# Optimization experiments

Hardware: AMD Instinct MI355X
Metric: run time of the kernel (lower is better)

Reference implementation:

```python
import jax, jax.numpy as jnp
import numpy as np

ALPHA = 1.702  # ORT swiglu activation constant


def setup_inputs() -> dict:
    key = jax.random.key(0)
    ks = jax.random.split(key, 6)
    B, S, H, I, E = 4, 1024, 2048, 2048, 8
    return {
        "hidden_states": jax.random.normal(ks[0], (B, S, H), dtype=jnp.float32),
        "gate_w": jax.random.normal(ks[1], (E, H), dtype=jnp.float32) * 0.02,
        "fc1_w": jax.random.normal(ks[2], (E, 2 * I, H), dtype=jnp.float32) * 0.02,
        "fc1_b": jax.random.normal(ks[3], (E, 2 * I), dtype=jnp.float32) * 0.02,
        "fc2_w": jax.random.normal(ks[4], (E, H, I), dtype=jnp.float32) * 0.02,
        "fc2_b": jax.random.normal(ks[5], (E, H), dtype=jnp.float32) * 0.02,
        "top_k": 2,
    }


def reference(hidden_states, gate_w, fc1_w, fc1_b, fc2_w, fc2_b, top_k):
    B, S, H = hidden_states.shape
    E = gate_w.shape[0]
    x = hidden_states.reshape(-1, H)                      # [T, H]
    T = x.shape[0]

    # Router: softmax -> top-k -> renormalize selected weights
    logits = jnp.einsum("th,eh->te", x, gate_w)           # [T, E]
    probs = jax.nn.softmax(logits, axis=-1)
    top_vals, top_idx = jax.lax.top_k(probs, top_k)       # [T, k]
    top_vals = top_vals / jnp.sum(top_vals, axis=-1, keepdims=True)
    # Dense combine weights [T, E] (zero for non-selected experts)
    combine = jnp.zeros((T, E), dtype=x.dtype).at[
        jnp.arange(T)[:, None], top_idx
    ].add(top_vals)

    # Expert FC1 (packed gate/linear, interleaved) -> swiglu -> FC2
    h = jnp.einsum("th,efh->etf", x, fc1_w) + fc1_b[:, None, :]   # [E, T, 2I]
    g = h[..., 0::2]                                              # gate part [E, T, I]
    l = h[..., 1::2]                                              # linear part [E, T, I]
    a = g * jax.nn.sigmoid(ALPHA * g) * (l + 1.0)                 # [E, T, I]
    y = jnp.einsum("eti,ehi->eth", a, fc2_w) + fc2_b[:, None, :]  # [E, T, H]

    out = jnp.einsum("te,eth->th", combine, y)            # weighted combine
    return out.reshape(B, S, H)
```

## Files before the change

### kernel.cpp

```cpp
#include <hip/hip_runtime.h>
#include <math.h>


#define T_TOK 4096
#define H_DIM 2048
#define I_DIM 2048
#define F_DIM 4096
#define E_NUM 8
#define ALPHA_C 1.702f
#define ALPHA_LOG2E 2.4554674f

#define TILE_M 64
#define KT 32
#define ACT_CAP_F (2 * T_TOK + E_NUM * TILE_M)
#define BTM 128
#define ACT_CAP_B (2 * T_TOK + E_NUM * BTM)

#define GATE_BLOCKS (T_TOK / 4)
#define CHUNK_F4 2048
#define NCHUNK 12288
#define W1_CHUNKS 8192
#define W1_F4 16777216
#define CVT_BLOCKS 2048
#define CVT_ITERS (NCHUNK / CVT_BLOCKS)

typedef unsigned short ushort_t;
typedef __attribute__((ext_vector_type(8))) unsigned short ushort8v;
typedef __attribute__((ext_vector_type(8))) __bf16 bf16x8;
typedef __attribute__((ext_vector_type(4))) float f32x4;

__device__ __forceinline__ ushort_t f2bf(float f) {
    unsigned int u = __float_as_uint(f);
    unsigned int r = (u + 0x7FFFu + ((u >> 16) & 1u)) >> 16;
    return (ushort_t)r;
}
__device__ __forceinline__ float bf2f(ushort_t b) {
    return __uint_as_float(((unsigned int)b) << 16);
}

__device__ __forceinline__ void gl_lds16(const ushort_t* g, ushort_t* l) {
    __builtin_amdgcn_global_load_lds(
        (const __attribute__((address_space(1))) void*)g,
        (__attribute__((address_space(3))) void*)l, 16, 0, 0);
}

__global__ __launch_bounds__(256) void gate_kernel(
    const float* __restrict__ x, const float* __restrict__ gw,
    ushort_t* __restrict__ xb, int4* __restrict__ tidx,
    float2* __restrict__ twgt) {
    int t = blockIdx.x * 4 + (threadIdx.x >> 6);
    int lane = threadIdx.x & 63;
    const float* xr = x + (size_t)t * H_DIM;
    ushort_t* xbr = xb + (size_t)t * H_DIM;
    float acc[E_NUM];
#pragma unroll
    for (int e = 0; e < E_NUM; e++) acc[e] = 0.f;
#pragma unroll
    for (int i = 0; i < H_DIM / 256; i++) {
        int j = (i * 64 + lane) * 4;
        float4 xv = *(const float4*)(xr + j);
        *(ushort4*)(xbr + j) =
            make_ushort4(f2bf(xv.x), f2bf(xv.y), f2bf(xv.z), f2bf(xv.w));
#pragma unroll
        for (int e = 0; e < E_NUM; e++) {
            float4 g = *(const float4*)(gw + e * H_DIM + j);
            acc[e] += xv.x * g.x + xv.y * g.y + xv.z * g.z + xv.w * g.w;
        }
    }
#pragma unroll
    for (int e = 0; e < E_NUM; e++) {
#pragma unroll
        for (int s = 32; s > 0; s >>= 1) acc[e] += __shfl_xor(acc[e], s, 64);
    }
    if (lane == 0) {
        int i0 = 0; float b0 = acc[0];
        for (int e = 1; e < E_NUM; e++) if (acc[e] > b0) { b0 = acc[e]; i0 = e; }
        int i1 = -1; float b1 = -3.0e38f;
        for (int e = 0; e < E_NUM; e++) {
            if (e == i0) continue;
            if (acc[e] > b1) { b1 = acc[e]; i1 = e; }
        }
        float e10 = expf(b1 - b0);
        float w0 = 1.f / (1.f + e10);
        float w1v = 1.f - w0;
        tidx[t] = make_int4(i0, 0, i1, 0);
        twgt[t] = make_float2(w0, w1v);
    }
}

__global__ __launch_bounds__(256) void route_kernel(
    const int4* tidx_ro, int* tidx_w, int* __restrict__ tok,
    int* __restrict__ cnt) {
    int e = blockIdx.x;
    int tid = threadIdx.x;
    int lane = tid & 63;
    int wv = tid >> 6;
    __shared__ int wsum[4];
    __shared__ int sbase;
    if (tid == 0) sbase = 0;
    __syncthreads();
    for (int c = 0; c < T_TOK / 256; c++) {
        int t = c * 256 + tid;
        int4 v = tidx_ro[t];
        bool fA = (v.x == e);
        bool fB = (v.z == e);
        bool f = fA || fB;
        unsigned long long m = __ballot(f);
        int my = __popcll(m & ((1ull << lane) - 1ull));
        int wt = __popcll(m);
        if (lane == 0) wsum[wv] = wt;
        __syncthreads();
        int woff = 0;
#pragma unroll
        for (int q = 0; q < 4; q++) woff += (q < wv) ? wsum[q] : 0;
        int tot = wsum[0] + wsum[1] + wsum[2] + wsum[3];
        int base = sbase;
        if (f) {
            int p = base + woff + my;
            tok[e * T_TOK + p] = t;
            tidx_w[t * 4 + (fA ? 1 : 3)] = p;
        }
        __syncthreads();
        if (tid == 0) sbase = base + tot;
        __syncthreads();
    }
    if (tid == 0) cnt[e] = sbase;
}

__global__ __launch_bounds__(256) void cvt_kernel(
    const float* __restrict__ w1, const float* __restrict__ w2,
    ushort_t* __restrict__ wb) {
    int bid = (int)blockIdx.x;
    int tid = (int)threadIdx.x;
    for (int i = 0; i < CVT_ITERS; i++) {
        int c = bid + i * CVT_BLOCKS;
        size_t g0 = (size_t)c * CHUNK_F4 + tid;
        const float* s = (c < W1_CHUNKS)
                             ? (w1 + g0 * 4)
                             : (w2 + (g0 - (size_t)W1_F4) * 4);
        ushort_t* d = wb + g0 * 4;
        f32x4 v[8];
#pragma unroll
        for (int j = 0; j < 8; j++)
            v[j] = *(const f32x4*)(s + (size_t)j * 1024);
#pragma unroll
        for (int j = 0; j < 8; j++) {
            *(ushort4*)(d + (size_t)j * 1024) = make_ushort4(
                f2bf(v[j][0]), f2bf(v[j][1]), f2bf(v[j][2]), f2bf(v[j][3]));
        }
    }
}

__device__ __forceinline__ void calc_off(const int* __restrict__ cnt, int e,
                                         int& off_e, int& cpad_e) {
    int o = 0, cp = 0;
#pragma unroll
    for (int q = 0; q < E_NUM; q++) {
        int c = (cnt[q] + BTM - 1) & ~(BTM - 1);
        if (q < e) o += c;
        if (q == e) cp = c;
    }
    off_e = o; cpad_e = cp;
}

__global__ __launch_bounds__(256, 3) void fc1_mfma(
    const ushort_t* __restrict__ xb, const ushort_t* __restrict__ w1b,
    const float* __restrict__ b1, const int* __restrict__ tok,
    const int* __restrict__ cnt, ushort_t* __restrict__ act) {
    int e = blockIdx.y >> 5;
    int tile = blockIdx.y & 31;
    int off_e, cpad_e;
    calc_off(cnt, e, off_e, cpad_e);
    if (tile * BTM >= cpad_e) return;
    int i0 = blockIdx.x * 64;

    __shared__ ushort_t As[2][128 * 32];
    __shared__ ushort_t Bg[2][64 * 32];
    __shared__ ushort_t Bl[2][64 * 32];

    int tid = threadIdx.x;
    int lane = tid & 63;
    int ww = tid >> 6;
    int wm = ww & 1, wn = ww >> 1;
    int l15 = lane & 15, quad = lane >> 4;
    int r4 = lane >> 2;
    int koff = (lane & 3) * 8;

    const int* tlist = tok + e * T_TOK + tile * BTM;
    int ar0 = ww * 32 + r4;
    const ushort_t* a0 = xb + (size_t)tlist[ar0] * H_DIM + koff;
    const ushort_t* a1 = xb + (size_t)tlist[ar0 + 16] * H_DIM + koff;
    int il = ww * 16 + r4;
    const ushort_t* bsrc = w1b + ((size_t)e * F_DIM + 2 * (i0 + il)) * H_DIM + koff;

    ushort_t* ad0a = &As[0][(ww * 32) * 32];
    ushort_t* ad0b = &As[0][(ww * 32 + 16) * 32];
    ushort_t* ad1a = &As[1][(ww * 32) * 32];
    ushort_t* ad1b = &As[1][(ww * 32 + 16) * 32];
    ushort_t* bg0 = &Bg[0][(ww * 16) * 32];
    ushort_t* bg1 = &Bg[1][(ww * 16) * 32];
    ushort_t* bl0 = &Bl[0][(ww * 16) * 32];
    ushort_t* bl1 = &Bl[1][(ww * 16) * 32];

    f32x4 zf = {0.f, 0.f, 0.f, 0.f};
    f32x4 accg[4][2], accl[4][2];
#pragma unroll
    for (int mc = 0; mc < 4; mc++)
#pragma unroll
        for (int nc = 0; nc < 2; nc++) { accg[mc][nc] = zf; accl[mc][nc] = zf; }

    for (int k0 = 0; k0 < H_DIM; k0 += 64) {
        __syncthreads();
        gl_lds16(a0, ad0a);
        gl_lds16(a1, ad0b);
        gl_lds16(a0 + 32, ad1a);
        gl_lds16(a1 + 32, ad1b);
        gl_lds16(bsrc, bg0);
        gl_lds16(bsrc + 32, bg1);
        gl_lds16(bsrc + H_DIM, bl0);
        gl_lds16(bsrc + H_DIM + 32, bl1);
        a0 += 64; a1 += 64; bsrc += 64;
        __syncthreads();

#pragma unroll
        for (int kk = 0; kk < 2; kk++) {
            bf16x8 af[4], bgf[2], blf[2];
#pragma unroll
            for (int mc = 0; mc < 4; mc++)
                af[mc] = *(const bf16x8*)&As[kk][(wm * 64 + mc * 16 + l15) * 32 + quad * 8];
#pragma unroll
            for (int nc = 0; nc < 2; nc++) {
                bgf[nc] = *(const bf16x8*)&Bg[kk][(wn * 32 + nc * 16 + l15) * 32 + quad * 8];
                blf[nc] = *(const bf16x8*)&Bl[kk][(wn * 32 + nc * 16 + l15) * 32 + quad * 8];
            }
#pragma unroll
            for (int mc = 0; mc < 4; mc++)
#pragma unroll
                for (int nc = 0; nc < 2; nc++) {
                    accg[mc][nc] = __builtin_amdgcn_mfma_f32_16x16x32_bf16(
                        af[mc], bgf[nc], accg[mc][nc], 0, 0, 0);
                    accl[mc][nc] = __builtin_amdgcn_mfma_f32_16x16x32_bf16(
                        af[mc], blf[nc], accl[mc][nc], 0, 0, 0);
                }
        }
    }

    int rowbase = off_e + tile * BTM + wm * 64;
    int colbase = i0 + wn * 32;
    float bgc[2], blc[2];
#pragma unroll
    for (int nc = 0; nc < 2; nc++) {
        int i = colbase + nc * 16 + l15;
        bgc[nc] = b1[(size_t)e * F_DIM + 2 * i];
        blc[nc] = b1[(size_t)e * F_DIM + 2 * i + 1];
    }
#pragma unroll
    for (int mc = 0; mc < 4; mc++)
#pragma unroll
        for (int nc = 0; nc < 2; nc++) {
            int i = colbase + nc * 16 + l15;
#pragma unroll
            for (int r = 0; r < 4; r++) {
                int m = rowbase + mc * 16 + quad * 4 + r;
                float g = accg[mc][nc][r] + bgc[nc];
                float l = accl[mc][nc][r] + blc[nc];
                float s = __builtin_amdgcn_rcpf(
                    1.f + __builtin_amdgcn_exp2f(-ALPHA_LOG2E * g));
                act[(size_t)m * I_DIM + i] = f2bf(g * s * (l + 1.f));
            }
        }
}

__global__ __launch_bounds__(256, 3) void fc2_mfma(
    const ushort_t* __restrict__ act, const ushort_t* __restrict__ w2b,
    const float* __restrict__ b2, const int* __restrict__ cnt,
    ushort_t* __restrict__ ybuf) {
    int e = blockIdx.y >> 5;
    int tile = blockIdx.y & 31;
    int off_e, cpad_e;
    calc_off(cnt, e, off_e, cpad_e);
    if (tile * BTM >= cpad_e) return;
    int h0 = blockIdx.x * 128;
    int rowbase = off_e + tile * BTM;

    __shared__ ushort_t As[2][128 * 32];
    __shared__ ushort_t Bs[2][128 * 32];

    int tid = threadIdx.x;
    int lane = tid & 63;
    int ww = tid >> 6;
    int wm = ww & 1, wn = ww >> 1;
    int l15 = lane & 15, quad = lane >> 4;
    int r4 = lane >> 2;
    int koff = (lane & 3) * 8;

    int ar = ww * 32 + r4;
    const ushort_t* a0 = act + (size_t)(rowbase + ar) * I_DIM + koff;
    const ushort_t* a1 = a0 + (size_t)16 * I_DIM;
    const ushort_t* b0 = w2b + ((size_t)e * H_DIM + h0 + ar) * I_DIM + koff;
    const ushort_t* b1p = b0 + (size_t)16 * I_DIM;

    ushort_t* ad0a = &As[0][(ww * 32) * 32];
    ushort_t* ad0b = &As[0][(ww * 32 + 16) * 32];
    ushort_t* ad1a = &As[1][(ww * 32) * 32];
    ushort_t* ad1b = &As[1][(ww * 32 + 16) * 32];
    ushort_t* bd0a = &Bs[0][(ww * 32) * 32];
    ushort_t* bd0b = &Bs[0][(ww * 32 + 16) * 32];
    ushort_t* bd1a = &Bs[1][(ww * 32) * 32];
    ushort_t* bd1b = &Bs[1][(ww * 32 + 16) * 32];

    f32x4 zf = {0.f, 0.f, 0.f, 0.f};
    f32x4 acc[4][4];
#pragma unroll
    for (int mc = 0; mc < 4; mc++)
#pragma unroll
        for (int nc = 0; nc < 4; nc++) acc[mc][nc] = zf;

    for (int k0 = 0; k0 < I_DIM; k0 += 64) {
        __syncthreads();
        gl_lds16(a0, ad0a);
        gl_lds16(a1, ad0b);
        gl_lds16(a0 + 32, ad1a);
        gl_lds16(a1 + 32, ad1b);
        gl_lds16(b0, bd0a);
        gl_lds16(b1p, bd0b);
        gl_lds16(b0 + 32, bd1a);
        gl_lds16(b1p + 32, bd1b);
        a0 += 64; a1 += 64; b0 += 64; b1p += 64;
        __syncthreads();

#pragma unroll
        for (int kk = 0; kk < 2; kk++) {
            bf16x8 af[4], bf[4];
#pragma unroll
            for (int mc = 0; mc < 4; mc++)
                af[mc] = *(const bf16x8*)&As[kk][(wm * 64 + mc * 16 + l15) * 32 + quad * 8];
#pragma unroll
            for (int nc = 0; nc < 4; nc++)
                bf[nc] = *(const bf16x8*)&Bs[kk][(wn * 64 + nc * 16 + l15) * 32 + quad * 8];
#pragma unroll
            for (int mc = 0; mc < 4; mc++)
#pragma unroll
                for (int nc = 0; nc < 4; nc++)
                    acc[mc][nc] = __builtin_amdgcn_mfma_f32_16x16x32_bf16(
                        af[mc], bf[nc], acc[mc][nc], 0, 0, 0);
        }
    }

    float bc[4];
#pragma unroll
    for (int nc = 0; nc < 4; nc++)
        bc[nc] = b2[(size_t)e * H_DIM + h0 + wn * 64 + nc * 16 + l15];
#pragma unroll
    for (int mc = 0; mc < 4; mc++)
#pragma unroll
        for (int nc = 0; nc < 4; nc++) {
            int h = h0 + wn * 64 + nc * 16 + l15;
#pragma unroll
            for (int r = 0; r < 4; r++) {
                int m = rowbase + wm * 64 + mc * 16 + quad * 4 + r;
                ybuf[(size_t)m * H_DIM + h] = f2bf(acc[mc][nc][r] + bc[nc]);
            }
        }
}

__global__ __launch_bounds__(256) void combine_kernel(
    const ushort_t* __restrict__ ybuf, const int4* __restrict__ tidx,
    const float2* __restrict__ twgt, const int* __restrict__ cnt,
    float* __restrict__ out) {
    int offv[E_NUM];
    {
        int o = 0;
#pragma unroll
        for (int q = 0; q < E_NUM; q++) {
            offv[q] = o;
            o += (cnt[q] + BTM - 1) & ~(BTM - 1);
        }
    }
    int h = threadIdx.x * 8;
#pragma unroll
    for (int tt = 0; tt < 4; tt++) {
        int t = blockIdx.x * 4 + tt;
        int4 idx = tidx[t];
        float2 w = twgt[t];
        size_t r0 = (size_t)offv[idx.x] + idx.y;
        size_t r1 = (size_t)offv[idx.z] + idx.w;
        ushort8v a = *(const ushort8v*)(ybuf + r0 * H_DIM + h);
        ushort8v b = *(const ushort8v*)(ybuf + r1 * H_DIM + h);
        float* op = out + (size_t)t * H_DIM + h;
#pragma unroll
        for (int q = 0; q < 8; q++)
            op[q] = w.x * bf2f(a[q]) + w.y * bf2f(b[q]);
    }
}

__global__ __launch_bounds__(64) void gate_fb(
    const float* __restrict__ x, const float* __restrict__ gw,
    int* __restrict__ tok, float* __restrict__ wgt,
    int4* __restrict__ tidx, float2* __restrict__ twgt, int* __restrict__ cnt) {
    int t = blockIdx.x;
    int lane = threadIdx.x;
    const float* xr = x + (size_t)t * H_DIM;
    float acc[E_NUM];
#pragma unroll
    for (int e = 0; e < E_NUM; e++) acc[e] = 0.f;
    for (int j = lane; j < H_DIM; j += 64) {
        float xv = xr[j];
#pragma unroll
        for (int e = 0; e < E_NUM; e++) acc[e] += xv * gw[e * H_DIM + j];
    }
#pragma unroll
    for (int e = 0; e < E_NUM; e++) {
#pragma unroll
        for (int s = 32; s > 0; s >>= 1) acc[e] += __shfl_xor(acc[e], s, 64);
    }
    if (lane == 0) {
        int i0 = 0; float b0 = acc[0];
        for (int e = 1; e < E_NUM; e++) if (acc[e] > b0) { b0 = acc[e]; i0 = e; }
        int i1 = -1; float b1 = -3.0e38f;
        for (int e = 0; e < E_NUM; e++) {
            if (e == i0) continue;
            if (acc[e] > b1) { b1 = acc[e]; i1 = e; }
        }
        float e10 = expf(b1 - b0);
        float w0 = 1.f / (1.f + e10);
        float w1 = 1.f - w0;
        int p0 = atomicAdd(&cnt[i0], 1);
        tok[i0 * T_TOK + p0] = t; wgt[i0 * T_TOK + p0] = w0;
        int p1 = atomicAdd(&cnt[i1], 1);
        tok[i1 * T_TOK + p1] = t; wgt[i1 * T_TOK + p1] = w1;
        tidx[t] = make_int4(i0, p0, i1, p1);
        twgt[t] = make_float2(w0, w1);
    }
}

__global__ __launch_bounds__(256) void pad_kernel(
    int* __restrict__ tok, float* __restrict__ wgt,
    const int* __restrict__ cnt, int* __restrict__ cnt_pad,
    int* __restrict__ off, int tile) {
    __shared__ int s_cnt[E_NUM], s_pad[E_NUM];
    if (threadIdx.x == 0) {
        int o = 0;
        for (int e = 0; e < E_NUM; e++) {
            int c = cnt[e];
            int cp = (c + tile - 1) / tile * tile;
            s_cnt[e] = c; s_pad[e] = cp;
            cnt_pad[e] = cp;
            off[e] = o;
            o += cp;
        }
    }
    __syncthreads();
    for (int e = 0; e < E_NUM; e++) {
        for (int p = s_cnt[e] + (int)threadIdx.x; p < s_pad[e]; p += 256) {
            tok[e * T_TOK + p] = 0;
            wgt[e * T_TOK + p] = 0.f;
        }
    }
}

__global__ __launch_bounds__(256) void fc1_kernel(
    const float* __restrict__ x, const float* __restrict__ w1,
    const float* __restrict__ b1, const int* __restrict__ tok,
    const int* __restrict__ cnt_pad, const int* __restrict__ off,
    ushort_t* __restrict__ act) {
    int e = blockIdx.y >> 6;
    int tile = blockIdx.y & 63;
    if (tile * TILE_M >= cnt_pad[e]) return;
    int i0 = blockIdx.x * 64;
    int f0 = i0 * 2;

    __shared__ float xs[KT][TILE_M + 4];
    __shared__ float wsh[KT][128 + 4];

    int tid = threadIdx.x;
    int tx = tid & 15, ty = tid >> 4;
    int rloc = tid >> 3;
    int c4 = (tid & 7) * 4;

    const int* tlist = tok + e * T_TOK + tile * TILE_M;
    int tk0 = tlist[rloc];
    int tk1 = tlist[rloc + 32];
    const float* xp0 = x + (size_t)tk0 * H_DIM + c4;
    const float* xp1 = x + (size_t)tk1 * H_DIM + c4;
    const float* wp = w1 + ((size_t)e * F_DIM + f0 + rloc) * H_DIM + c4;

    float ga[4][4] = {{0.f}}, la[4][4] = {{0.f}};

    for (int k0 = 0; k0 < H_DIM; k0 += KT) {
        __syncthreads();
        {
            float4 v0 = *(const float4*)(xp0 + k0);
            float4 v1 = *(const float4*)(xp1 + k0);
            xs[c4 + 0][rloc] = v0.x; xs[c4 + 1][rloc] = v0.y;
            xs[c4 + 2][rloc] = v0.z; xs[c4 + 3][rloc] = v0.w;
            xs[c4 + 0][rloc + 32] = v1.x; xs[c4 + 1][rloc + 32] = v1.y;
            xs[c4 + 2][rloc + 32] = v1.z; xs[c4 + 3][rloc + 32] = v1.w;
        }
        {
#pragma unroll
            for (int r = 0; r < 4; r++) {
                float4 v = *(const float4*)(wp + (size_t)(32 * r) * H_DIM + k0);
                int fr = rloc + 32 * r;
                wsh[c4 + 0][fr] = v.x; wsh[c4 + 1][fr] = v.y;
                wsh[c4 + 2][fr] = v.z; wsh[c4 + 3][fr] = v.w;
            }
        }
        __syncthreads();
#pragma unroll
        for (int k = 0; k < KT; k++) {
            float4 xv = *(const float4*)&xs[k][ty * 4];
            float4 wa = *(const float4*)&wsh[k][tx * 8];
            float4 wb = *(const float4*)&wsh[k][tx * 8 + 4];
            float xm[4] = {xv.x, xv.y, xv.z, xv.w};
            float gg[4] = {wa.x, wa.z, wb.x, wb.z};
            float ll[4] = {wa.y, wa.w, wb.y, wb.w};
#pragma unroll
            for (int m = 0; m < 4; m++)
#pragma unroll
                for (int n = 0; n < 4; n++) {
                    ga[m][n] += xm[m] * gg[n];
                    la[m][n] += xm[m] * ll[n];
                }
        }
    }

    int rowbase = off[e] + tile * TILE_M;
    float bg[4], bl[4];
#pragma unroll
    for (int n = 0; n < 4; n++) {
        int i = i0 + tx * 4 + n;
        bg[n] = b1[(size_t)e * F_DIM + 2 * i];
        bl[n] = b1[(size_t)e * F_DIM + 2 * i + 1];
    }
#pragma unroll
    for (int m = 0; m < 4; m++) {
        int row = rowbase + ty * 4 + m;
        ushort_t us[4];
#pragma unroll
        for (int n = 0; n < 4; n++) {
            float g = ga[m][n] + bg[n];
            float l = la[m][n] + bl[n];
            float s = 1.f / (1.f + expf(-ALPHA_C * g));
            us[n] = f2bf(g * s * (l + 1.f));
        }
        *(ushort4*)&act[(size_t)row * I_DIM + i0 + tx * 4] =
            make_ushort4(us[0], us[1], us[2], us[3]);
    }
}

__global__ __launch_bounds__(256) void fc2_kernel(
    const ushort_t* __restrict__ act, const float* __restrict__ w2,
    const float* __restrict__ b2, const int* __restrict__ tok,
    const float* __restrict__ wgt, const int* __restrict__ cnt_pad,
    const int* __restrict__ off, float* __restrict__ out) {
    int e = blockIdx.y >> 6;
    int tile = blockIdx.y & 63;
    if (tile * TILE_M >= cnt_pad[e]) return;
    int h0 = blockIdx.x * 64;

    __shared__ float as_[KT][TILE_M + 4];
    __shared__ float wsh[KT][64 + 4];

    int tid = threadIdx.x;
    int tx = tid & 15, ty = tid >> 4;
    int rowbase = off[e] + tile * TILE_M;

    int arow = tid >> 2;
    int ac8 = (tid & 3) * 8;
    const ushort_t* ap = act + (size_t)(rowbase + arow) * I_DIM + ac8;
    int rloc = tid >> 3;
    int c4 = (tid & 7) * 4;
    const float* wp = w2 + ((size_t)e * H_DIM + h0 + rloc) * I_DIM + c4;

    float acc[4][4] = {{0.f}};

    for (int k0 = 0; k0 < I_DIM; k0 += KT) {
        __syncthreads();
        {
            ushort8v v = *(const ushort8v*)(ap + k0);
#pragma unroll
            for (int q = 0; q < 8; q++) as_[ac8 + q][arow] = bf2f(v[q]);
        }
        {
#pragma unroll
            for (int r = 0; r < 2; r++) {
                float4 v = *(const float4*)(wp + (size_t)(32 * r) * I_DIM + k0);
                int hr = rloc + 32 * r;
                wsh[c4 + 0][hr] = v.x; wsh[c4 + 1][hr] = v.y;
                wsh[c4 + 2][hr] = v.z; wsh[c4 + 3][hr] = v.w;
            }
        }
        __syncthreads();
#pragma unroll
        for (int k = 0; k < KT; k++) {
            float4 xv = *(const float4*)&as_[k][ty * 4];
            float4 wv = *(const float4*)&wsh[k][tx * 4];
            float xm[4] = {xv.x, xv.y, xv.z, xv.w};
            float wn[4] = {wv.x, wv.y, wv.z, wv.w};
#pragma unroll
            for (int m = 0; m < 4; m++)
#pragma unroll
                for (int n = 0; n < 4; n++) acc[m][n] += xm[m] * wn[n];
        }
    }

    const int* tlist = tok + e * T_TOK + tile * TILE_M;
    const float* wlist = wgt + e * T_TOK + tile * TILE_M;
#pragma unroll
    for (int m = 0; m < 4; m++) {
        int row = ty * 4 + m;
        int t = tlist[row];
        float w = wlist[row];
        if (w == 0.f) continue;
#pragma unroll
        for (int n = 0; n < 4; n++) {
            int h = h0 + tx * 4 + n;
            float y = acc[m][n] + b2[(size_t)e * H_DIM + h];
            atomicAdd(out + (size_t)t * H_DIM + h, w * y);
        }
    }
}

extern "C" void kernel_launch(void* const* d_in, const int* in_sizes, int n_in,
                              void* d_out, int out_size, void* d_ws, size_t ws_size,
                              hipStream_t stream) {
    const float* x  = (const float*)d_in[0];
    const float* gw = (const float*)d_in[1];
    const float* w1 = (const float*)d_in[2];
    const float* b1 = (const float*)d_in[3];
    const float* w2 = (const float*)d_in[4];
    const float* b2 = (const float*)d_in[5];
    float* out = (float*)d_out;
    char* ws = (char*)d_ws;

    size_t w1b_sz = (size_t)E_NUM * F_DIM * H_DIM * 2;
    size_t w2b_sz = (size_t)E_NUM * H_DIM * I_DIM * 2;
    size_t xb_sz  = (size_t)T_TOK * H_DIM * 2;
    size_t act_sz = (size_t)ACT_CAP_B * I_DIM * 2;
    size_t tok_sz = (size_t)E_NUM * T_TOK * 4;
    size_t tidx_sz = (size_t)T_TOK * 16;
    size_t twgt_sz = (size_t)T_TOK * 8;
    size_t need_big = w1b_sz + w2b_sz + xb_sz + act_sz + tok_sz + 64 +
                      tidx_sz + twgt_sz + 256;

    if (ws_size >= need_big) {
        ushort_t* w1b = (ushort_t*)ws;
        ushort_t* w2b = (ushort_t*)(ws + w1b_sz);
        ushort_t* xb  = (ushort_t*)(ws + w1b_sz + w2b_sz);
        ushort_t* act = (ushort_t*)(ws + w1b_sz + w2b_sz + xb_sz);
        char* p = ws + w1b_sz + w2b_sz + xb_sz + act_sz;
        int*    tok  = (int*)p;                 p += tok_sz;
        int*    cnt  = (int*)p;                 p += 64;
        int4*   tidx = (int4*)p;                p += tidx_sz;
        float2* twgt = (float2*)p;
        ushort_t* ybuf = w1b;

        hipMemsetAsync(tok, 0, tok_sz + 64, stream);
        gate_kernel<<<GATE_BLOCKS, 256, 0, stream>>>(x, gw, xb, tidx, twgt);
        route_kernel<<<E_NUM, 256, 0, stream>>>(
            (const int4*)tidx, (int*)tidx, tok, cnt);
        cvt_kernel<<<CVT_BLOCKS, 256, 0, stream>>>(w1, w2, w1b);
        fc1_mfma<<<dim3(I_DIM / 64, E_NUM * 32), 256, 0, stream>>>(
            xb, w1b, b1, tok, cnt, act);
        fc2_mfma<<<dim3(H_DIM / 128, E_NUM * 32), 256, 0, stream>>>(
            act, w2b, b2, cnt, ybuf);
        combine_kernel<<<T_TOK / 4, 256, 0, stream>>>(ybuf, tidx, twgt, cnt, out);
        return;
    }

    size_t actB = (size_t)ACT_CAP_F * I_DIM * 2;
    ushort_t* act = (ushort_t*)ws;
    char* p = ws + actB;
    int*    tok  = (int*)p;     p += tok_sz;
    float*  wgt  = (float*)p;   p += tok_sz;
    int4*   tidx = (int4*)p;    p += tidx_sz;
    float2* twgt = (float2*)p;  p += twgt_sz;
    int*    cnt  = (int*)p;
    int*    cnt_pad = cnt + E_NUM;
    int*    off  = cnt_pad + E_NUM;
    size_t need = actB + 2 * tok_sz + tidx_sz + twgt_sz + 256;
    if (ws_size < need) return;

    hipMemsetAsync(cnt, 0, E_NUM * sizeof(int), stream);
    hipMemsetAsync(d_out, 0, (size_t)T_TOK * H_DIM * sizeof(float), stream);
    gate_fb<<<T_TOK, 64, 0, stream>>>(x, gw, tok, wgt, tidx, twgt, cnt);
    pad_kernel<<<1, 256, 0, stream>>>(tok, wgt, cnt, cnt_pad, off, TILE_M);
    fc1_kernel<<<dim3(I_DIM / 64, E_NUM * 64), 256, 0, stream>>>(
        x, w1, b1, tok, cnt_pad, off, act);
    fc2_kernel<<<dim3(H_DIM / 64, E_NUM * 64), 256, 0, stream>>>(
        act, w2, b2, tok, wgt, cnt_pad, off, out);
}
```

Baseline: 791.3 us.

## Fuse weight conversion into gate and fc1 kernels and compact tile grid

Removes the standalone weight-conversion kernel. W1 fp32-to-bf16 conversion now runs as extra blocks of the gate kernel, and W2 conversion runs as extra column blocks of the fc1 kernel, so these bandwidth-bound copies can overlap with routing and GEMM work. The fc1 and fc2 grids switch from a fixed 32 tiles per expert to a compact padded-row tile count, and each block looks up its expert from its row offset, which cuts the number of early-exiting blocks. The cost is that conversion blocks compete with GEMM blocks for CUs and bandwidth.

```diff
diff --git a/kernel.cpp b/kernel.cpp
--- a/kernel.cpp
+++ b/kernel.cpp
@@ -15,14 +15,15 @@
 #define ACT_CAP_F (2 * T_TOK + E_NUM * TILE_M)
 #define BTM 128
 #define ACT_CAP_B (2 * T_TOK + E_NUM * BTM)
+#define TILES_Y (ACT_CAP_B / BTM)
 
 #define GATE_BLOCKS (T_TOK / 4)
 #define CHUNK_F4 2048
-#define NCHUNK 12288
 #define W1_CHUNKS 8192
-#define W1_F4 16777216
-#define CVT_BLOCKS 2048
-#define CVT_ITERS (NCHUNK / CVT_BLOCKS)
+#define CVT1_BLOCKS 2048
+#define CVT1_ITERS 4
+#define W2_CHUNKS 4096
+#define W2X 16
 
 typedef unsigned short ushort_t;
 typedef __attribute__((ext_vector_type(8))) unsigned short ushort8v;
@@ -44,10 +45,35 @@
         (__attribute__((address_space(3))) void*)l, 16, 0, 0);
 }
 
+__device__ __forceinline__ void cvt_chunk(const float* __restrict__ s,
+                                          ushort_t* __restrict__ d) {
+    f32x4 v[8];
+#pragma unroll
+    for (int j = 0; j < 8; j++)
+        v[j] = *(const f32x4*)(s + (size_t)j * 1024);
+#pragma unroll
+    for (int j = 0; j < 8; j++) {
+        *(ushort4*)(d + (size_t)j * 1024) = make_ushort4(
+            f2bf(v[j][0]), f2bf(v[j][1]), f2bf(v[j][2]), f2bf(v[j][3]));
+    }
+}
+
 __global__ __launch_bounds__(256) void gate_kernel(
     const float* __restrict__ x, const float* __restrict__ gw,
+    const float* __restrict__ w1, ushort_t* __restrict__ w1b,
     ushort_t* __restrict__ xb, int4* __restrict__ tidx,
     float2* __restrict__ twgt) {
+    if (blockIdx.x >= GATE_BLOCKS) {
+        int bid = (int)blockIdx.x - GATE_BLOCKS;
+        int tid = (int)threadIdx.x;
+#pragma unroll
+        for (int i = 0; i < CVT1_ITERS; i++) {
+            int c = bid + i * CVT1_BLOCKS;
+            size_t g0 = (size_t)c * CHUNK_F4 + tid;
+            cvt_chunk(w1 + g0 * 4, w1b + g0 * 4);
+        }
+        return;
+    }
     int t = blockIdx.x * 4 + (threadIdx.x >> 6);
     int lane = threadIdx.x & 63;
     const float* xr = x + (size_t)t * H_DIM;
@@ -127,51 +153,38 @@
     if (tid == 0) cnt[e] = sbase;
 }
 
-__global__ __launch_bounds__(256) void cvt_kernel(
-    const float* __restrict__ w1, const float* __restrict__ w2,
-    ushort_t* __restrict__ wb) {
-    int bid = (int)blockIdx.x;
-    int tid = (int)threadIdx.x;
-    for (int i = 0; i < CVT_ITERS; i++) {
-        int c = bid + i * CVT_BLOCKS;
-        size_t g0 = (size_t)c * CHUNK_F4 + tid;
-        const float* s = (c < W1_CHUNKS)
-                             ? (w1 + g0 * 4)
-                             : (w2 + (g0 - (size_t)W1_F4) * 4);
-        ushort_t* d = wb + g0 * 4;
-        f32x4 v[8];
-#pragma unroll
-        for (int j = 0; j < 8; j++)
-            v[j] = *(const f32x4*)(s + (size_t)j * 1024);
-#pragma unroll
-        for (int j = 0; j < 8; j++) {
-            *(ushort4*)(d + (size_t)j * 1024) = make_ushort4(
-                f2bf(v[j][0]), f2bf(v[j][1]), f2bf(v[j][2]), f2bf(v[j][3]));
-        }
-    }
-}
-
-__device__ __forceinline__ void calc_off(const int* __restrict__ cnt, int e,
-                                         int& off_e, int& cpad_e) {
-    int o = 0, cp = 0;
+__device__ __forceinline__ bool find_tile(const int* __restrict__ cnt,
+                                          int row0, int& e, int& off_e,
+                                          int& cpad_e) {
+    int o = 0;
+    e = -1;
 #pragma unroll
     for (int q = 0; q < E_NUM; q++) {
         int c = (cnt[q] + BTM - 1) & ~(BTM - 1);
-        if (q < e) o += c;
-        if (q == e) cp = c;
-    }
-    off_e = o; cpad_e = cp;
+        if (row0 >= o && row0 < o + c) { e = q; off_e = o; cpad_e = c; }
+        o += c;
+    }
+    return e >= 0;
 }
 
 __global__ __launch_bounds__(256, 3) void fc1_mfma(
     const ushort_t* __restrict__ xb, const ushort_t* __restrict__ w1b,
     const float* __restrict__ b1, const int* __restrict__ tok,
-    const int* __restrict__ cnt, ushort_t* __restrict__ act) {
-    int e = blockIdx.y >> 5;
-    int tile = blockIdx.y & 31;
-    int off_e, cpad_e;
-    calc_off(cnt, e, off_e, cpad_e);
-    if (tile * BTM >= cpad_e) return;
+    const int* __restrict__ cnt, ushort_t* __restrict__ act,
+    const float* __restrict__ w2f, ushort_t* __restrict__ w2b) {
+    if (blockIdx.x >= I_DIM / 64) {
+        int flat = ((int)blockIdx.x - I_DIM / 64) * TILES_Y + (int)blockIdx.y;
+        int tid = (int)threadIdx.x;
+        for (int c = flat; c < W2_CHUNKS; c += W2X * TILES_Y) {
+            size_t g0 = (size_t)c * CHUNK_F4 + tid;
+            cvt_chunk(w2f + g0 * 4, w2b + g0 * 4);
+        }
+        return;
+    }
+    int row0 = (int)blockIdx.y * BTM;
+    int e, off_e, cpad_e;
+    if (!find_tile(cnt, row0, e, off_e, cpad_e)) return;
+    int tile = (row0 - off_e) / BTM;
     int i0 = blockIdx.x * 64;
 
     __shared__ ushort_t As[2][128 * 32];
@@ -245,7 +258,7 @@
         }
     }
 
-    int rowbase = off_e + tile * BTM + wm * 64;
+    int rowbase = row0 + wm * 64;
     int colbase = i0 + wn * 32;
     float bgc[2], blc[2];
 #pragma unroll
@@ -275,13 +288,11 @@
     const ushort_t* __restrict__ act, const ushort_t* __restrict__ w2b,
     const float* __restrict__ b2, const int* __restrict__ cnt,
     ushort_t* __restrict__ ybuf) {
-    int e = blockIdx.y >> 5;
-    int tile = blockIdx.y & 31;
-    int off_e, cpad_e;
-    calc_off(cnt, e, off_e, cpad_e);
-    if (tile * BTM >= cpad_e) return;
+    int row0 = (int)blockIdx.y * BTM;
+    int e, off_e, cpad_e;
+    if (!find_tile(cnt, row0, e, off_e, cpad_e)) return;
     int h0 = blockIdx.x * 128;
-    int rowbase = off_e + tile * BTM;
+    int rowbase = row0;
 
     __shared__ ushort_t As[2][128 * 32];
     __shared__ ushort_t Bs[2][128 * 32];
@@ -657,13 +668,13 @@
         ushort_t* ybuf = w1b;
 
         hipMemsetAsync(tok, 0, tok_sz + 64, stream);
-        gate_kernel<<<GATE_BLOCKS, 256, 0, stream>>>(x, gw, xb, tidx, twgt);
+        gate_kernel<<<GATE_BLOCKS + CVT1_BLOCKS, 256, 0, stream>>>(
+            x, gw, w1, w1b, xb, tidx, twgt);
         route_kernel<<<E_NUM, 256, 0, stream>>>(
             (const int4*)tidx, (int*)tidx, tok, cnt);
-        cvt_kernel<<<CVT_BLOCKS, 256, 0, stream>>>(w1, w2, w1b);
-        fc1_mfma<<<dim3(I_DIM / 64, E_NUM * 32), 256, 0, stream>>>(
-            xb, w1b, b1, tok, cnt, act);
-        fc2_mfma<<<dim3(H_DIM / 128, E_NUM * 32), 256, 0, stream>>>(
+        fc1_mfma<<<dim3(I_DIM / 64 + W2X, TILES_Y), 256, 0, stream>>>(
+            xb, w1b, b1, tok, cnt, act, w2, w2b);
+        fc2_mfma<<<dim3(H_DIM / 128, TILES_Y), 256, 0, stream>>>(
             act, w2b, b2, cnt, ybuf);
         combine_kernel<<<T_TOK / 4, 256, 0, stream>>>(ybuf, tidx, twgt, cnt, out);
         return;
```

New measurement: 765.9 us. -3.2%, faster.
